# Kernel tuning notes

Hardware: AMD Instinct MI355X
Metric: run time of the kernel (lower is better)

## Reference

```python
import jax, jax.numpy as jnp
import numpy as np

N_GRAPHS = 128
N_NODES = 512
N = N_GRAPHS * N_NODES      # 65536 total nodes
E = 524288                  # edges (avg degree 8)
F_IN = 4                    # num_features
EMB = 4                     # embedding_dim
HEADS = 4
GDIM = 16                   # GATConv_dim
D = GDIM * HEADS            # 64 = d_model
NHEAD = 2                   # heads // 2
FF = 64                     # ff_hid_dim
OUT = 64                    # output_dim
N_GAT_REST = 3              # gat_layers - 1


def setup_inputs() -> dict:
    key = jax.random.key(0)
    ks = iter(jax.random.split(key, 64))
    def nrm(shape, fan_in):
        return jax.random.normal(next(ks), shape, jnp.float32) / np.float32(np.sqrt(fan_in))
    inp = {}
    inp['x'] = jax.random.normal(next(ks), (N, F_IN), jnp.float32)
    inp['edge_index'] = jax.random.randint(next(ks), (2, E), 0, N, dtype=jnp.int32)
    inp['batch'] = jnp.repeat(jnp.arange(N_GRAPHS, dtype=jnp.int32), N_NODES)
    # feature_fc
    inp['Wf'] = nrm((F_IN, EMB), F_IN); inp['bf'] = jnp.zeros((EMB,), jnp.float32)
    # input GATConv (EMB -> HEADS*GDIM)
    inp['gW0'] = nrm((EMB, HEADS * GDIM), EMB)
    inp['aS0'] = nrm((HEADS, GDIM), GDIM); inp['aD0'] = nrm((HEADS, GDIM), GDIM)
    inp['gb0'] = jnp.zeros((D,), jnp.float32)
    # remaining 3 GATConv layers (D -> HEADS*GDIM), stacked
    inp['gW'] = nrm((N_GAT_REST, D, HEADS * GDIM), D)
    inp['aS'] = nrm((N_GAT_REST, HEADS, GDIM), GDIM); inp['aD'] = nrm((N_GAT_REST, HEADS, GDIM), GDIM)
    inp['gb'] = jnp.zeros((N_GAT_REST, D), jnp.float32)
    # decoder layer: self-attn, cross-attn, layernorms, FFN
    for p in ['sWq','sWk','sWv','sWo','cWq','cWk','cWv','cWo']:
        inp[p] = nrm((D, D), D)
    for p in ['sbq','sbk','sbv','sbo','cbq','cbk','cbv','cbo']:
        inp[p] = jnp.zeros((D,), jnp.float32)
    for g, b in [('ln1g','ln1b'), ('ln2g','ln2b'), ('ln3g','ln3b')]:
        inp[g] = jnp.ones((D,), jnp.float32); inp[b] = jnp.zeros((D,), jnp.float32)
    inp['ffW1'] = nrm((D, FF), D); inp['ffb1'] = jnp.zeros((FF,), jnp.float32)
    inp['ffW2'] = nrm((FF, D), FF); inp['ffb2'] = jnp.zeros((D,), jnp.float32)
    inp['fcW'] = nrm((D, OUT), D); inp['fcb'] = jnp.zeros((OUT,), jnp.float32)
    return inp


def _gat(h_in, src, dst, W, a_s, a_d, b):
    # PyG GATConv, concat=True, negative_slope=0.2, self-loops already in (src,dst)
    h = (h_in @ W).reshape(N, HEADS, GDIM)
    es = jnp.einsum('nho,ho->nh', h, a_s)   # [N,H]
    ed = jnp.einsum('nho,ho->nh', h, a_d)
    e = jax.nn.leaky_relu(es[src] + ed[dst], 0.2)          # [E',H]
    m = jax.ops.segment_max(e, dst, num_segments=N)        # segment softmax over dst
    w = jnp.exp(e - m[dst])
    s = jax.ops.segment_sum(w, dst, num_segments=N)
    alpha = w / (s[dst] + 1e-16)
    out = jax.ops.segment_sum(h[src] * alpha[..., None], dst, num_segments=N)
    return out.reshape(N, D) + b


def _mha(q, kv, Wq, bq, Wk, bk, Wv, bv, Wo, bo):
    B, S, Dm = q.shape
    hd = Dm // NHEAD
    Q = (q @ Wq + bq).reshape(B, S, NHEAD, hd)
    K = (kv @ Wk + bk).reshape(B, S, NHEAD, hd)
    V = (kv @ Wv + bv).reshape(B, S, NHEAD, hd)
    a = jax.nn.softmax(jnp.einsum('bqhd,bkhd->bhqk', Q, K) / jnp.sqrt(jnp.float32(hd)), axis=-1)
    o = jnp.einsum('bhqk,bkhd->bqhd', a, V).reshape(B, S, Dm)
    return o @ Wo + bo


def _ln(x, g, b):
    m = x.mean(-1, keepdims=True)
    v = ((x - m) ** 2).mean(-1, keepdims=True)
    return (x - m) / jnp.sqrt(v + 1e-5) * g + b


def reference(x, edge_index, batch, Wf, bf, gW0, aS0, aD0, gb0, gW, aS, aD, gb,
              sWq, sWk, sWv, sWo, cWq, cWk, cWv, cWo,
              sbq, sbk, sbv, sbo, cbq, cbk, cbv, cbo,
              ln1g, ln1b, ln2g, ln2b, ln3g, ln3b,
              ffW1, ffb1, ffW2, ffb2, fcW, fcb):
    loops = jnp.arange(N, dtype=edge_index.dtype)
    src = jnp.concatenate([edge_index[0], loops])
    dst = jnp.concatenate([edge_index[1], loops])
    h = x @ Wf + bf
    h = jax.nn.leaky_relu(_gat(h, src, dst, gW0, aS0, aD0, gb0), 0.01)
    for i in range(N_GAT_REST):
        h = jax.nn.leaky_relu(_gat(h, src, dst, gW[i], aS[i], aD[i], gb[i]), 0.01)
    t = h.reshape(N_GRAPHS, N_NODES, D)
    # one transformer decoder layer, post-norm, memory = layer input
    mem = t
    t = _ln(t + _mha(t, t, sWq, sbq, sWk, sbk, sWv, sbv, sWo, sbo), ln1g, ln1b)
    t = _ln(t + _mha(t, mem, cWq, cbq, cWk, cbk, cWv, cbv, cWo, cbo), ln2g, ln2b)
    t = _ln(t + (jax.nn.relu(t @ ffW1 + ffb1) @ ffW2 + ffb2), ln3g, ln3b)
    h = t.reshape(N, D)
    pooled = jax.ops.segment_sum(h, batch, num_segments=N_GRAPHS) / jnp.float32(N_NODES)
    return pooled @ fcW + fcb
```

## Files before the change

kernel.cpp:

```cpp
#include <hip/hip_runtime.h>
#include <math.h>

#define NG 128
#define SEQ 512
#define NN 65536
#define EE 524288
#define DM 64
#define HSTR 80

typedef __attribute__((ext_vector_type(8))) short short8;
typedef __attribute__((ext_vector_type(4))) short short4v;
typedef __attribute__((ext_vector_type(4))) float f32x4;

__device__ __forceinline__ float lrelu(float x, float s){ return x > 0.f ? x : s*x; }

__device__ __forceinline__ unsigned short f2bf(float x){
  union { float f; unsigned u; } v; v.f = x;
  unsigned r = v.u + 0x7FFF + ((v.u>>16)&1);
  return (unsigned short)(r>>16);
}
__device__ __forceinline__ float bf2f(unsigned short x){
  union { unsigned u; float f; } v; v.u = ((unsigned)x)<<16;
  return v.f;
}

__global__ void k_count(const int* __restrict__ dst, int* __restrict__ deg){
  int e = blockIdx.x*256 + threadIdx.x;
  atomicAdd(&deg[dst[e]], 1);
}

__global__ void k_scan1(const int* __restrict__ deg, int* __restrict__ excl, int* __restrict__ bsums){
  __shared__ int sm[256];
  int tid = threadIdx.x;
  int i = blockIdx.x*256 + tid;
  int v = deg[i];
  sm[tid] = v;
  __syncthreads();
  int val = v;
  for (int off=1; off<256; off<<=1){
    int add = (tid>=off)? sm[tid-off] : 0;
    __syncthreads();
    val += add;
    sm[tid] = val;
    __syncthreads();
  }
  excl[i] = val - v;
  if (tid==255) bsums[blockIdx.x] = val;
}

__global__ void k_scan2(int* __restrict__ bsums){
  __shared__ int sm[256];
  int tid=threadIdx.x;
  int v = bsums[tid];
  sm[tid]=v;
  __syncthreads();
  int val=v;
  for (int off=1; off<256; off<<=1){
    int add = (tid>=off)? sm[tid-off]:0;
    __syncthreads();
    val += add;
    sm[tid]=val;
    __syncthreads();
  }
  bsums[tid] = val - v;
}

__global__ void k_scan3(const int* __restrict__ excl, const int* __restrict__ bsums,
                        int* __restrict__ rowp, int* __restrict__ cursor){
  int i = blockIdx.x*256 + threadIdx.x;
  int v = excl[i] + bsums[blockIdx.x];
  rowp[i]=v; cursor[i]=v;
  if (i==0) rowp[NN]=EE;
}

__global__ void k_fill(const int* __restrict__ src, const int* __restrict__ dst,
                       int* __restrict__ cursor, int* __restrict__ col){
  int e = blockIdx.x*256 + threadIdx.x;
  int d = dst[e];
  int p = atomicAdd(&cursor[d], 1);
  col[p] = src[e];
}

__global__ void __launch_bounds__(256) k_transform0(const float* __restrict__ x,
                            const float* __restrict__ Wf, const float* __restrict__ bf,
                            const float* __restrict__ gW0,
                            const float* __restrict__ aSp, const float* __restrict__ aDp,
                            unsigned short* __restrict__ hout, float* __restrict__ ed){
  __shared__ float inL[4][68];
  __shared__ float Wl[4][64];
  __shared__ float b0l[64];
  __shared__ float asl[64], adl[64];
  int tid = threadIdx.x;
  int n0 = blockIdx.x*64;
  if (tid < 64){
    asl[tid] = aSp[tid]; adl[tid] = aDp[tid];
    float b = 0.f;
    #pragma unroll
    for (int k=0;k<4;k++) b += bf[k]*gW0[k*64+tid];
    b0l[tid] = b;
  }
  {
    int i = tid>>6, j = tid&63;
    float s = 0.f;
    #pragma unroll
    for (int k=0;k<4;k++) s += Wf[i*4+k]*gW0[k*64+j];
    Wl[i][j] = s;
  }
  if (tid < 64){
    float4 v = *(const float4*)&x[(size_t)(n0+tid)*4];
    inL[0][tid]=v.x; inL[1][tid]=v.y; inL[2][tid]=v.z; inL[3][tid]=v.w;
  }
  __syncthreads();
  int i = tid>>4, j = tid&15;
  float acc[4][4];
  #pragma unroll
  for (int r=0;r<4;r++){
    #pragma unroll
    for (int c=0;c<4;c++) acc[r][c] = 0.f;
  }
  #pragma unroll
  for (int k=0;k<4;k++){
    float4 av = *(float4*)&inL[k][4*i];
    float4 bv = *(float4*)&Wl[k][4*j];
    float a_[4]={av.x,av.y,av.z,av.w}, b_[4]={bv.x,bv.y,bv.z,bv.w};
    #pragma unroll
    for (int r=0;r<4;r++){
      #pragma unroll
      for (int c=0;c<4;c++) acc[r][c] += a_[r]*b_[c];
    }
  }
  float4 asv = *(float4*)&asl[4*j];
  float4 adv = *(float4*)&adl[4*j];
  float4 bbv = *(float4*)&b0l[4*j];
  float bb[4] = {bbv.x, bbv.y, bbv.z, bbv.w};
  #pragma unroll
  for (int r=0;r<4;r++){
    float y0=acc[r][0]+bb[0], y1=acc[r][1]+bb[1], y2=acc[r][2]+bb[2], y3=acc[r][3]+bb[3];
    int node = n0 + 4*i + r;
    ushort4 hv;
    hv.x=f2bf(y0); hv.y=f2bf(y1); hv.z=f2bf(y2); hv.w=f2bf(y3);
    *(ushort4*)&hout[(size_t)node*HSTR + 4*j] = hv;
    float ps = y0*asv.x + y1*asv.y + y2*asv.z + y3*asv.w;
    float pd = y0*adv.x + y1*adv.y + y2*adv.z + y3*adv.w;
    ps += __shfl_xor(ps,1); ps += __shfl_xor(ps,2);
    pd += __shfl_xor(pd,1); pd += __shfl_xor(pd,2);
    if ((j&3)==0){
      *(float*)&hout[(size_t)node*HSTR + 64 + 2*(j>>2)] = ps;
      ed[(size_t)node*4 + (j>>2)] = pd;
    }
  }
}

__global__ void __launch_bounds__(256) k_transform_bf(const unsigned short* __restrict__ hin, const float* __restrict__ W,
                            const float* __restrict__ aSp, const float* __restrict__ aDp,
                            unsigned short* __restrict__ hout, float* __restrict__ ed){
  __shared__ float inL[64][68];
  __shared__ float Wl[64][64];
  __shared__ float asl[64], adl[64];
  int tid = threadIdx.x;
  int n0 = blockIdx.x*64;
  if (tid < 64){ asl[tid] = aSp[tid]; adl[tid] = aDp[tid]; }
  for (int idx=tid; idx<1024; idx+=256){
    int k = idx>>4, jj = (idx&15)<<2;
    *(float4*)&Wl[k][jj] = *(const float4*)&W[k*64+jj];
  }
  for (int idx=tid; idx<1024; idx+=256){
    int node = idx>>4, kk = (idx&15)<<2;
    ushort4 v = *(const ushort4*)&hin[(size_t)(n0+node)*64 + kk];
    inL[kk][node]=bf2f(v.x); inL[kk+1][node]=bf2f(v.y); inL[kk+2][node]=bf2f(v.z); inL[kk+3][node]=bf2f(v.w);
  }
  __syncthreads();
  int i = tid>>4, j = tid&15;
  float acc[4][4];
  #pragma unroll
  for (int r=0;r<4;r++){
    #pragma unroll
    for (int c=0;c<4;c++) acc[r][c] = 0.f;
  }
  #pragma unroll 4
  for (int k=0;k<64;k++){
    float4 av = *(float4*)&inL[k][4*i];
    float4 bv = *(float4*)&Wl[k][4*j];
    float a_[4]={av.x,av.y,av.z,av.w}, b_[4]={bv.x,bv.y,bv.z,bv.w};
    #pragma unroll
    for (int r=0;r<4;r++){
      #pragma unroll
      for (int c=0;c<4;c++) acc[r][c] += a_[r]*b_[c];
    }
  }
  float4 asv = *(float4*)&asl[4*j];
  float4 adv = *(float4*)&adl[4*j];
  #pragma unroll
  for (int r=0;r<4;r++){
    float y0=acc[r][0], y1=acc[r][1], y2=acc[r][2], y3=acc[r][3];
    int node = n0 + 4*i + r;
    ushort4 hv;
    hv.x=f2bf(y0); hv.y=f2bf(y1); hv.z=f2bf(y2); hv.w=f2bf(y3);
    *(ushort4*)&hout[(size_t)node*HSTR + 4*j] = hv;
    float ps = y0*asv.x + y1*asv.y + y2*asv.z + y3*asv.w;
    float pd = y0*adv.x + y1*adv.y + y2*adv.z + y3*adv.w;
    ps += __shfl_xor(ps,1); ps += __shfl_xor(ps,2);
    pd += __shfl_xor(pd,1); pd += __shfl_xor(pd,2);
    if ((j&3)==0){
      *(float*)&hout[(size_t)node*HSTR + 64 + 2*(j>>2)] = ps;
      ed[(size_t)node*4 + (j>>2)] = pd;
    }
  }
}

template<int BF16OUT>
__global__ void __launch_bounds__(256) k_aggregate(const unsigned short* __restrict__ h,
                            const float* __restrict__ ed, const int* __restrict__ rowp,
                            const int* __restrict__ col, const float* __restrict__ gb,
                            void* __restrict__ houtv){
  int tid = threadIdx.x;
  int n = blockIdx.x*4 + (tid>>6);
  int l = tid&63;
  int q = l>>4;
  int sl = l&15;
  int head = sl>>2;
  float edn = ed[(size_t)n*4 + head];
  float es_self = *(const float*)&h[(size_t)n*HSTR + 64 + 2*head];
  int beg = __builtin_amdgcn_readfirstlane(rowp[n]);
  int end = __builtin_amdgcn_readfirstlane(rowp[n+1]);
  float m = -1e30f, s = 0.f;
  float a0=0.f, a1=0.f, a2=0.f, a3=0.f;
  int i = beg;
  for (; i+8 <= end; i += 8){
    int c0=col[i], c1=col[i+1], c2=col[i+2], c3=col[i+3];
    int c4=col[i+4], c5=col[i+5], c6=col[i+6], c7=col[i+7];
    int t01 = (q&1)? c1 : c0;
    int t23 = (q&1)? c3 : c2;
    int sq0 = (q&2)? t23 : t01;
    int t45 = (q&1)? c5 : c4;
    int t67 = (q&1)? c7 : c6;
    int sq1 = (q&2)? t67 : t45;
    size_t b0r = (size_t)sq0*HSTR, b1r = (size_t)sq1*HSTR;
    ushort4 hv0 = *(const ushort4*)&h[b0r + 4*sl];
    ushort4 hv1 = *(const ushort4*)&h[b1r + 4*sl];
    float e0 = lrelu(*(const float*)&h[b0r + 64 + 2*head] + edn, 0.2f);
    float e1 = lrelu(*(const float*)&h[b1r + 64 + 2*head] + edn, 0.2f);
    float mx = fmaxf(e0, e1);
    if (__any(mx > m + 8.f)){
      float nm = fmaxf(m, mx);
      float c = __expf(m - nm);
      s*=c; a0*=c; a1*=c; a2*=c; a3*=c; m = nm;
    }
    float w0 = __expf(e0 - m);
    float w1 = __expf(e1 - m);
    s += w0 + w1;
    a0 += w0*bf2f(hv0.x) + w1*bf2f(hv1.x);
    a1 += w0*bf2f(hv0.y) + w1*bf2f(hv1.y);
    a2 += w0*bf2f(hv0.z) + w1*bf2f(hv1.z);
    a3 += w0*bf2f(hv0.w) + w1*bf2f(hv1.w);
  }
  if (i < end){
    int last = end-1;
    int i1=(i+1<last)?i+1:last, i2=(i+2<last)?i+2:last, i3=(i+3<last)?i+3:last;
    int i4=(i+4<last)?i+4:last, i5=(i+5<last)?i+5:last, i6=(i+6<last)?i+6:last;
    int c0=col[i], c1=col[i1], c2=col[i2], c3=col[i3];
    int c4=col[i4], c5=col[i5], c6=col[i6], c7=col[last];
    int t01 = (q&1)? c1 : c0;
    int t23 = (q&1)? c3 : c2;
    int sq0 = (q&2)? t23 : t01;
    int t45 = (q&1)? c5 : c4;
    int t67 = (q&1)? c7 : c6;
    int sq1 = (q&2)? t67 : t45;
    bool ac0 = (i + q) < end;
    bool ac1 = (i + 4 + q) < end;
    size_t b0r = (size_t)sq0*HSTR, b1r = (size_t)sq1*HSTR;
    ushort4 hv0 = *(const ushort4*)&h[b0r + 4*sl];
    ushort4 hv1 = *(const ushort4*)&h[b1r + 4*sl];
    float e0 = lrelu(*(const float*)&h[b0r + 64 + 2*head] + edn, 0.2f);
    float e1 = lrelu(*(const float*)&h[b1r + 64 + 2*head] + edn, 0.2f);
    if (!ac0) e0 = -1e30f;
    if (!ac1) e1 = -1e30f;
    float mx = fmaxf(e0, e1);
    if (__any(mx > m + 8.f)){
      float nm = fmaxf(m, mx);
      float c = __expf(m - nm);
      s*=c; a0*=c; a1*=c; a2*=c; a3*=c; m = nm;
    }
    float w0 = ac0 ? __expf(e0 - m) : 0.f;
    float w1 = ac1 ? __expf(e1 - m) : 0.f;
    s += w0 + w1;
    a0 += w0*bf2f(hv0.x) + w1*bf2f(hv1.x);
    a1 += w0*bf2f(hv0.y) + w1*bf2f(hv1.y);
    a2 += w0*bf2f(hv0.z) + w1*bf2f(hv1.z);
    a3 += w0*bf2f(hv0.w) + w1*bf2f(hv1.w);
  }
  #pragma unroll
  for (int off=16; off<=32; off<<=1){
    float m2 = __shfl_xor(m, off);
    float s2 = __shfl_xor(s, off);
    float b0 = __shfl_xor(a0, off);
    float b1 = __shfl_xor(a1, off);
    float b2 = __shfl_xor(a2, off);
    float b3 = __shfl_xor(a3, off);
    float nm = fmaxf(m, m2);
    float c1 = __expf(m - nm), c2 = __expf(m2 - nm);
    s  = s*c1  + s2*c2;
    a0 = a0*c1 + b0*c2;
    a1 = a1*c1 + b1*c2;
    a2 = a2*c1 + b2*c2;
    a3 = a3*c1 + b3*c2;
    m = nm;
  }
  {
    float e_self = lrelu(es_self + edn, 0.2f);
    float nm = fmaxf(m, e_self);
    float c = __expf(m - nm), cs = __expf(e_self - nm);
    ushort4 hs = *(const ushort4*)&h[(size_t)n*HSTR + 4*sl];
    s  = s*c  + cs;
    a0 = a0*c + cs*bf2f(hs.x);
    a1 = a1*c + cs*bf2f(hs.y);
    a2 = a2*c + cs*bf2f(hs.z);
    a3 = a3*c + cs*bf2f(hs.w);
  }
  if (q == 0){
    float inv = 1.f/(s + 1e-16f);
    float4 gv = *(const float4*)&gb[4*sl];
    float o0 = lrelu(a0*inv + gv.x, 0.01f);
    float o1 = lrelu(a1*inv + gv.y, 0.01f);
    float o2 = lrelu(a2*inv + gv.z, 0.01f);
    float o3 = lrelu(a3*inv + gv.w, 0.01f);
    if (BF16OUT){
      ushort4 hv; hv.x=f2bf(o0); hv.y=f2bf(o1); hv.z=f2bf(o2); hv.w=f2bf(o3);
      *(ushort4*)((unsigned short*)houtv + (size_t)n*64 + 4*sl) = hv;
    } else {
      *(float4*)((float*)houtv + (size_t)n*64 + 4*sl) = make_float4(o0,o1,o2,o3);
    }
  }
}

__global__ void __launch_bounds__(256) k_qkv3(const float* __restrict__ in0, const float* __restrict__ W0, const float* __restrict__ b0, unsigned short* __restrict__ o0,
                      const float* __restrict__ in1, const float* __restrict__ W1, const float* __restrict__ b1, unsigned short* __restrict__ o1,
                      const float* __restrict__ in2, const float* __restrict__ W2, const float* __restrict__ b2, unsigned short* __restrict__ o2,
                      float scl0){
  __shared__ float inL[64][68];
  __shared__ float Wl[64][64];
  int tid = threadIdx.x;
  int n0 = blockIdx.x*64;
  int i = tid>>4, j = tid&15;
  const float* ins[3] = {in0, in1, in2};
  const float* Ws[3] = {W0, W1, W2};
  const float* bs[3] = {b0, b1, b2};
  unsigned short* os[3] = {o0, o1, o2};
  const float* cur = nullptr;
  for (int w=0; w<3; w++){
    __syncthreads();
    if (ins[w] != cur){
      cur = ins[w];
      for (int idx=tid; idx<1024; idx+=256){
        int node = idx>>4, kk = (idx&15)<<2;
        float4 v = *(const float4*)&cur[(size_t)(n0+node)*64 + kk];
        inL[kk][node]=v.x; inL[kk+1][node]=v.y; inL[kk+2][node]=v.z; inL[kk+3][node]=v.w;
      }
    }
    for (int idx=tid; idx<1024; idx+=256){
      int k = idx>>4, jj = (idx&15)<<2;
      *(float4*)&Wl[k][jj] = *(const float4*)&Ws[w][k*64+jj];
    }
    __syncthreads();
    float acc[4][4];
    #pragma unroll
    for (int r=0;r<4;r++){
      #pragma unroll
      for (int c=0;c<4;c++) acc[r][c] = 0.f;
    }
    #pragma unroll 4
    for (int k=0;k<64;k++){
      float4 av = *(float4*)&inL[k][4*i];
      float4 bv = *(float4*)&Wl[k][4*j];
      float a_[4]={av.x,av.y,av.z,av.w}, b_[4]={bv.x,bv.y,bv.z,bv.w};
      #pragma unroll
      for (int r=0;r<4;r++){
        #pragma unroll
        for (int c=0;c<4;c++) acc[r][c] += a_[r]*b_[c];
      }
    }
    float4 bv = *(const float4*)&bs[w][4*j];
    float bb[4] = {bv.x, bv.y, bv.z, bv.w};
    float sc = (w==0) ? scl0 : 1.f;
    #pragma unroll
    for (int r=0;r<4;r++){
      ushort4 hv;
      hv.x = f2bf((acc[r][0]+bb[0])*sc);
      hv.y = f2bf((acc[r][1]+bb[1])*sc);
      hv.z = f2bf((acc[r][2]+bb[2])*sc);
      hv.w = f2bf((acc[r][3]+bb[3])*sc);
      *(ushort4*)&os[w][(size_t)(n0+4*i+r)*64 + 4*j] = hv;
    }
  }
}

__global__ void __launch_bounds__(256) k_ffn(const float* __restrict__ in,
                     const float* __restrict__ W1p, const float* __restrict__ b1p,
                     const float* __restrict__ W2p, const float* __restrict__ b2p,
                     const float* __restrict__ g, const float* __restrict__ bl,
                     float* __restrict__ out){
  __shared__ float inL[64][68];
  __shared__ float Wl[64][64];
  __shared__ float ffL[64][68];
  int tid = threadIdx.x;
  int n0 = blockIdx.x*64;
  for (int idx=tid; idx<1024; idx+=256){
    int k = idx>>4, jj = (idx&15)<<2;
    *(float4*)&Wl[k][jj] = *(const float4*)&W1p[k*64+jj];
  }
  for (int idx=tid; idx<1024; idx+=256){
    int node = idx>>4, kk = (idx&15)<<2;
    float4 v = *(const float4*)&in[(size_t)(n0+node)*64 + kk];
    inL[kk][node]=v.x; inL[kk+1][node]=v.y; inL[kk+2][node]=v.z; inL[kk+3][node]=v.w;
  }
  __syncthreads();
  int i = tid>>4, j = tid&15;
  float acc[4][4];
  #pragma unroll
  for (int r=0;r<4;r++){
    #pragma unroll
    for (int c=0;c<4;c++) acc[r][c] = 0.f;
  }
  #pragma unroll 4
  for (int k=0;k<64;k++){
    float4 av = *(float4*)&inL[k][4*i];
    float4 bv = *(float4*)&Wl[k][4*j];
    float a_[4]={av.x,av.y,av.z,av.w}, b_[4]={bv.x,bv.y,bv.z,bv.w};
    #pragma unroll
    for (int r=0;r<4;r++){
      #pragma unroll
      for (int c=0;c<4;c++) acc[r][c] += a_[r]*b_[c];
    }
  }
  float4 b1v = *(const float4*)&b1p[4*j];
  float bb1[4] = {b1v.x, b1v.y, b1v.z, b1v.w};
  #pragma unroll
  for (int r=0;r<4;r++){
    #pragma unroll
    for (int c=0;c<4;c++){
      ffL[4*j+c][4*i+r] = fmaxf(acc[r][c] + bb1[c], 0.f);
    }
  }
  __syncthreads();
  for (int idx=tid; idx<1024; idx+=256){
    int k = idx>>4, jj = (idx&15)<<2;
    *(float4*)&Wl[k][jj] = *(const float4*)&W2p[k*64+jj];
  }
  __syncthreads();
  #pragma unroll
  for (int r=0;r<4;r++){
    #pragma unroll
    for (int c=0;c<4;c++) acc[r][c] = 0.f;
  }
  #pragma unroll 4
  for (int k=0;k<64;k++){
    float4 av = *(float4*)&ffL[k][4*i];
    float4 bv = *(float4*)&Wl[k][4*j];
    float a_[4]={av.x,av.y,av.z,av.w}, b_[4]={bv.x,bv.y,bv.z,bv.w};
    #pragma unroll
    for (int r=0;r<4;r++){
      #pragma unroll
      for (int c=0;c<4;c++) acc[r][c] += a_[r]*b_[c];
    }
  }
  float4 b2v = *(const float4*)&b2p[4*j];
  float bb2v[4] = {b2v.x, b2v.y, b2v.z, b2v.w};
  float4 gv = *(const float4*)&g[4*j];
  float4 blv = *(const float4*)&bl[4*j];
  float gg[4] = {gv.x, gv.y, gv.z, gv.w};
  float bbl[4] = {blv.x, blv.y, blv.z, blv.w};
  #pragma unroll
  for (int r=0;r<4;r++){
    int node = n0 + 4*i + r;
    float y[4];
    #pragma unroll
    for (int c=0;c<4;c++) y[c] = acc[r][c] + bb2v[c] + inL[4*j+c][4*i+r];
    float s = (y[0]+y[1]) + (y[2]+y[3]);
    s += __shfl_xor(s,1); s += __shfl_xor(s,2); s += __shfl_xor(s,4); s += __shfl_xor(s,8);
    float mean = s * (1.f/64.f);
    float d[4] = {y[0]-mean, y[1]-mean, y[2]-mean, y[3]-mean};
    float v = (d[0]*d[0]+d[1]*d[1]) + (d[2]*d[2]+d[3]*d[3]);
    v += __shfl_xor(v,1); v += __shfl_xor(v,2); v += __shfl_xor(v,4); v += __shfl_xor(v,8);
    float inv = rsqrtf(v*(1.f/64.f) + 1e-5f);
    *(float4*)&out[(size_t)node*64 + 4*j] =
      make_float4(d[0]*inv*gg[0]+bbl[0], d[1]*inv*gg[1]+bbl[1],
                  d[2]*inv*gg[2]+bbl[2], d[3]*inv*gg[3]+bbl[3]);
  }
}

__global__ void __launch_bounds__(512) k_attn_fused(const unsigned short* __restrict__ Q, const unsigned short* __restrict__ K,
                      const unsigned short* __restrict__ V,
                      const float* __restrict__ Wo, const float* __restrict__ bo,
                      const float* __restrict__ res, const float* __restrict__ g, const float* __restrict__ bl,
                      float* __restrict__ out){
  __shared__ __align__(16) char smem[40960];
  char* Ksm = smem;
  char* Vsm = smem + 16384;
  char* Psm = smem + 32768;

  int bid = blockIdx.x;
  int qq = bid & 3;
  int b  = bid >> 2;
  int tid = threadIdx.x;
  int wave = tid>>6;
  int l = tid & 63;
  int lq = l & 15;
  int g4 = l >> 4;
  int head = wave & 1;
  int qg = wave >> 1;
  const size_t gb = (size_t)b*SEQ*64;
  const int hoff = head*32;
  const f32x4 zero = {0.f,0.f,0.f,0.f};

  int qrow0 = qq*128 + qg*32;
  short8 qf[2];
  f32x4 O[2][2];
  float m_[2], l_[2];
  #pragma unroll
  for (int qt=0; qt<2; qt++){
    qf[qt] = *(const short8*)(Q + gb + (size_t)(qrow0 + qt*16 + lq)*64 + hoff + g4*8);
    O[qt][0] = zero; O[qt][1] = zero;
    m_[qt] = -1e30f; l_[qt] = 0.f;
  }
  char* Pw = Psm + wave*1024;

  for (int ph=0; ph<4; ph++){
    __syncthreads();
    #pragma unroll
    for (int it=0; it<2; it++){
      int idx = tid + it*512;
      int row = idx>>3, gr = idx&7;
      uint4 v = *(const uint4*)(K + gb + (size_t)(ph*128 + row)*64 + gr*8);
      *(uint4*)(Ksm + row*128 + ((gr*16) ^ ((row&7)<<4))) = v;
    }
    #pragma unroll
    for (int it=0; it<2; it++){
      int idx = tid + it*512;
      int key = idx>>3, gr = idx&7;
      uint4 vv = *(const uint4*)(V + gb + (size_t)(ph*128 + key)*64 + gr*8);
      const unsigned short* vs = (const unsigned short*)&vv;
      #pragma unroll
      for (int c=0;c<8;c++){
        int d = gr*8 + c;
        *(unsigned short*)(Vsm + d*256 + ((key*2) ^ ((d&7)<<4))) = vs[c];
      }
    }
    __syncthreads();
    for (int p=0; p<4; p++){
      int r0 = p*32 + lq, r1 = r0 + 16;
      short8 kf0 = *(short8*)(Ksm + r0*128 + ((hoff*2 + g4*16) ^ ((r0&7)<<4)));
      short8 kf1 = *(short8*)(Ksm + r1*128 + ((hoff*2 + g4*16) ^ ((r1&7)<<4)));
      int d0 = hoff + lq, d1 = hoff + lq + 16;
      short8 vt0 = *(short8*)(Vsm + d0*256 + ((p*64 + g4*16) ^ ((d0&7)<<4)));
      short8 vt1 = *(short8*)(Vsm + d1*256 + ((p*64 + g4*16) ^ ((d1&7)<<4)));
      int swzp = ((lq>>1)&3)<<4;
      #pragma unroll
      for (int qt=0; qt<2; qt++){
        f32x4 s0 = __builtin_amdgcn_mfma_f32_16x16x32_bf16(kf0, qf[qt], zero, 0,0,0);
        f32x4 s1 = __builtin_amdgcn_mfma_f32_16x16x32_bf16(kf1, qf[qt], zero, 0,0,0);
        float pmax = fmaxf(fmaxf(fmaxf(s0.x,s0.y),fmaxf(s0.z,s0.w)),
                           fmaxf(fmaxf(s1.x,s1.y),fmaxf(s1.z,s1.w)));
        pmax = fmaxf(pmax, __shfl_xor(pmax, 16));
        pmax = fmaxf(pmax, __shfl_xor(pmax, 32));
        float mn = fmaxf(m_[qt], pmax);
        float corr = __expf(m_[qt] - mn);
        m_[qt] = mn;
        float e0 = __expf(s0.x - mn), e1 = __expf(s0.y - mn);
        float e2 = __expf(s0.z - mn), e3 = __expf(s0.w - mn);
        float e4 = __expf(s1.x - mn), e5 = __expf(s1.y - mn);
        float e6 = __expf(s1.z - mn), e7 = __expf(s1.w - mn);
        l_[qt] = l_[qt]*corr + (((e0+e1)+(e2+e3)) + ((e4+e5)+(e6+e7)));
        O[qt][0] *= corr; O[qt][1] *= corr;
        uint2 w0, w1;
        w0.x = (unsigned)f2bf(e0) | ((unsigned)f2bf(e1)<<16);
        w0.y = (unsigned)f2bf(e2) | ((unsigned)f2bf(e3)<<16);
        w1.x = (unsigned)f2bf(e4) | ((unsigned)f2bf(e5)<<16);
        w1.y = (unsigned)f2bf(e6) | ((unsigned)f2bf(e7)<<16);
        *(uint2*)(Pw + lq*64 + ((g4*8) ^ swzp)) = w0;
        *(uint2*)(Pw + lq*64 + ((32 + g4*8) ^ swzp)) = w1;
        short8 pb = *(short8*)(Pw + lq*64 + ((g4*16) ^ swzp));
        O[qt][0] = __builtin_amdgcn_mfma_f32_16x16x32_bf16(vt0, pb, O[qt][0], 0,0,0);
        O[qt][1] = __builtin_amdgcn_mfma_f32_16x16x32_bf16(vt1, pb, O[qt][1], 0,0,0);
      }
    }
  }
  __syncthreads();
  unsigned short* OT = (unsigned short*)smem;
  float* WoL = (float*)(smem + 17664);
  #pragma unroll
  for (int qt=0; qt<2; qt++){
    float lt = l_[qt];
    lt += __shfl_xor(lt, 16);
    lt += __shfl_xor(lt, 32);
    float inv = 1.f/lt;
    int row = qg*32 + qt*16 + lq;
    #pragma unroll
    for (int c=0;c<4;c++){
      OT[(hoff + g4*4 + c)*136 + row]      = f2bf(O[qt][0][c]*inv);
      OT[(hoff + 16 + g4*4 + c)*136 + row] = f2bf(O[qt][1][c]*inv);
    }
  }
  for (int idx=tid; idx<1024; idx+=512){
    int k = idx>>4, jj = (idx&15)<<2;
    *(float4*)&WoL[k*64+jj] = *(const float4*)&Wo[k*64+jj];
  }
  __syncthreads();
  int i = tid>>4, j = tid&15;
  float acc[4][4];
  #pragma unroll
  for (int r=0;r<4;r++){
    #pragma unroll
    for (int c=0;c<4;c++) acc[r][c] = 0.f;
  }
  #pragma unroll 4
  for (int k=0;k<64;k++){
    short4v av = *(short4v*)&OT[k*136 + 4*i];
    float4 bv = *(float4*)&WoL[k*64 + 4*j];
    float b_[4]={bv.x,bv.y,bv.z,bv.w};
    #pragma unroll
    for (int r=0;r<4;r++){
      float a = bf2f((unsigned short)av[r]);
      #pragma unroll
      for (int c=0;c<4;c++) acc[r][c] += a*b_[c];
    }
  }
  float4 bov = *(const float4*)&bo[4*j];
  float4 gv = *(const float4*)&g[4*j];
  float4 blv = *(const float4*)&bl[4*j];
  float bb[4] = {bov.x, bov.y, bov.z, bov.w};
  float gg[4] = {gv.x, gv.y, gv.z, gv.w};
  float bbl[4] = {blv.x, blv.y, blv.z, blv.w};
  #pragma unroll
  for (int r=0;r<4;r++){
    int row = 4*i + r;
    int node = b*SEQ + qq*128 + row;
    float4 rv = *(const float4*)&res[(size_t)node*64 + 4*j];
    float y[4] = {acc[r][0]+bb[0]+rv.x, acc[r][1]+bb[1]+rv.y,
                  acc[r][2]+bb[2]+rv.z, acc[r][3]+bb[3]+rv.w};
    float s = (y[0]+y[1]) + (y[2]+y[3]);
    s += __shfl_xor(s,1); s += __shfl_xor(s,2); s += __shfl_xor(s,4); s += __shfl_xor(s,8);
    float mean = s * (1.f/64.f);
    float d[4] = {y[0]-mean, y[1]-mean, y[2]-mean, y[3]-mean};
    float v = (d[0]*d[0]+d[1]*d[1]) + (d[2]*d[2]+d[3]*d[3]);
    v += __shfl_xor(v,1); v += __shfl_xor(v,2); v += __shfl_xor(v,4); v += __shfl_xor(v,8);
    float inv = rsqrtf(v*(1.f/64.f) + 1e-5f);
    *(float4*)&out[(size_t)node*64 + 4*j] =
      make_float4(d[0]*inv*gg[0]+bbl[0], d[1]*inv*gg[1]+bbl[1],
                  d[2]*inv*gg[2]+bbl[2], d[3]*inv*gg[3]+bbl[3]);
  }
}

__global__ void __launch_bounds__(256) k_pool_fc(const float* __restrict__ t, const float* __restrict__ fcW,
                          const float* __restrict__ fcb, float* __restrict__ out){
  __shared__ float pl[4][64];
  __shared__ float pf[64];
  int b = blockIdx.x;
  int tid = threadIdx.x;
  int j = tid&63, seg = tid>>6;
  const float* basep = t + (size_t)b*SEQ*64;
  float s = 0.f;
  for (int si=seg*128; si<(seg+1)*128; si++) s += basep[(size_t)si*64 + j];
  pl[seg][j] = s;
  __syncthreads();
  if (tid < 64){
    pf[tid] = (pl[0][tid]+pl[1][tid]+pl[2][tid]+pl[3][tid]) * (1.f/512.f);
  }
  __syncthreads();
  if (tid < 64){
    float o = fcb[tid];
    for (int k=0;k<64;k++) o += pf[k]*fcW[k*64+tid];
    out[(size_t)b*64 + tid] = o;
  }
}

extern "C" void kernel_launch(void* const* d_in, const int* in_sizes, int n_in,
                              void* d_out, int out_size, void* d_ws, size_t ws_size,
                              hipStream_t stream) {
  const float* x    = (const float*)d_in[0];
  const int*   ei   = (const int*)d_in[1];
  const float* Wf   = (const float*)d_in[3];
  const float* bf   = (const float*)d_in[4];
  const float* gW0  = (const float*)d_in[5];
  const float* aS0  = (const float*)d_in[6];
  const float* aD0  = (const float*)d_in[7];
  const float* gb0  = (const float*)d_in[8];
  const float* gW   = (const float*)d_in[9];
  const float* aS   = (const float*)d_in[10];
  const float* aD   = (const float*)d_in[11];
  const float* gb   = (const float*)d_in[12];
  const float* sWq  = (const float*)d_in[13];
  const float* sWk  = (const float*)d_in[14];
  const float* sWv  = (const float*)d_in[15];
  const float* sWo  = (const float*)d_in[16];
  const float* cWq  = (const float*)d_in[17];
  const float* cWk  = (const float*)d_in[18];
  const float* cWv  = (const float*)d_in[19];
  const float* cWo  = (const float*)d_in[20];
  const float* sbq  = (const float*)d_in[21];
  const float* sbk  = (const float*)d_in[22];
  const float* sbv  = (const float*)d_in[23];
  const float* sbo  = (const float*)d_in[24];
  const float* cbq  = (const float*)d_in[25];
  const float* cbk  = (const float*)d_in[26];
  const float* cbv  = (const float*)d_in[27];
  const float* cbo  = (const float*)d_in[28];
  const float* ln1g = (const float*)d_in[29];
  const float* ln1b = (const float*)d_in[30];
  const float* ln2g = (const float*)d_in[31];
  const float* ln2b = (const float*)d_in[32];
  const float* ln3g = (const float*)d_in[33];
  const float* ln3b = (const float*)d_in[34];
  const float* ffW1 = (const float*)d_in[35];
  const float* ffb1 = (const float*)d_in[36];
  const float* ffW2 = (const float*)d_in[37];
  const float* ffb2 = (const float*)d_in[38];
  const float* fcW  = (const float*)d_in[39];
  const float* fcb  = (const float*)d_in[40];

  char* ws = (char*)d_ws;
  size_t off = 0;
  auto alloc = [&](size_t bytes) -> void* {
    void* p = ws + off;
    off += (bytes + 255) & ~(size_t)255;
    return p;
  };
  int* deg    = (int*)alloc(NN*sizeof(int));
  int* excl   = (int*)alloc(NN*sizeof(int));
  int* rowp   = (int*)alloc((NN+1)*sizeof(int));
  int* cursor = (int*)alloc(NN*sizeof(int));
  int* col    = (int*)alloc(EE*sizeof(int));
  int* bsums  = (int*)alloc(256*sizeof(int));
  float* ed   = (float*)alloc((size_t)NN*4*sizeof(float));
  unsigned short* Hb   = (unsigned short*)alloc((size_t)NN*HSTR*sizeof(unsigned short));
  unsigned short* Hagg = (unsigned short*)alloc((size_t)NN*64*sizeof(unsigned short));
  unsigned short* Qb = (unsigned short*)alloc((size_t)NN*64*sizeof(unsigned short));
  unsigned short* Kb = (unsigned short*)alloc((size_t)NN*64*sizeof(unsigned short));
  unsigned short* Vb = (unsigned short*)alloc((size_t)NN*64*sizeof(unsigned short));
  float* B1   = (float*)alloc((size_t)NN*64*sizeof(float));
  float* B2   = (float*)alloc((size_t)NN*64*sizeof(float));
  float* B5   = (float*)alloc((size_t)NN*64*sizeof(float));

  const int* e_src = ei;
  const int* e_dst = ei + EE;

  const float scale = 0.17677669529663687f;

  hipMemsetAsync(deg, 0, NN*sizeof(int), stream);
  k_count<<<EE/256, 256, 0, stream>>>(e_dst, deg);
  k_scan1<<<NN/256, 256, 0, stream>>>(deg, excl, bsums);
  k_scan2<<<1, 256, 0, stream>>>(bsums);
  k_scan3<<<NN/256, 256, 0, stream>>>(excl, bsums, rowp, cursor);
  k_fill<<<EE/256, 256, 0, stream>>>(e_src, e_dst, cursor, col);

  k_transform0<<<NN/64, 256, 0, stream>>>(x, Wf, bf, gW0, aS0, aD0, Hb, ed);
  k_aggregate<1><<<NN/4, 256, 0, stream>>>(Hb, ed, rowp, col, gb0, Hagg);
  k_transform_bf<<<NN/64, 256, 0, stream>>>(Hagg, gW+0*4096, aS+0*64, aD+0*64, Hb, ed);
  k_aggregate<1><<<NN/4, 256, 0, stream>>>(Hb, ed, rowp, col, gb+0*64, Hagg);
  k_transform_bf<<<NN/64, 256, 0, stream>>>(Hagg, gW+1*4096, aS+1*64, aD+1*64, Hb, ed);
  k_aggregate<1><<<NN/4, 256, 0, stream>>>(Hb, ed, rowp, col, gb+1*64, Hagg);
  k_transform_bf<<<NN/64, 256, 0, stream>>>(Hagg, gW+2*4096, aS+2*64, aD+2*64, Hb, ed);
  k_aggregate<0><<<NN/4, 256, 0, stream>>>(Hb, ed, rowp, col, gb+2*64, B2);

  k_qkv3<<<NN/64, 256, 0, stream>>>(B2, sWq, sbq, Qb, B2, sWk, sbk, Kb, B2, sWv, sbv, Vb, scale);
  k_attn_fused<<<NG*4, 512, 0, stream>>>(Qb, Kb, Vb, sWo, sbo, B2, ln1g, ln1b, B5);

  k_qkv3<<<NN/64, 256, 0, stream>>>(B5, cWq, cbq, Qb, B2, cWk, cbk, Kb, B2, cWv, cbv, Vb, scale);
  k_attn_fused<<<NG*4, 512, 0, stream>>>(Qb, Kb, Vb, cWo, cbo, B5, ln2g, ln2b, B2);

  k_ffn<<<NN/64, 256, 0, stream>>>(B2, ffW1, ffb1, ffW2, ffb2, ln3g, ln3b, B1);

  k_pool_fc<<<NG, 256, 0, stream>>>(B1, fcW, fcb, (float*)d_out);
}
```

Before: 409.1 us.

## Process 64-key blocks per softmax step with lazy max rescaling and new V swizzle

The flash-attention inner loop now handles 64 keys per online-softmax step instead of 32. This halves the number of max reductions and rescales. Rescaling of the running max is skipped unless some lane's new max exceeds the old one by more than 8, which removes most correction exps and multiplies. The V transpose swizzle and the P staging buffer are changed to reduce LDS bank conflicts, at the cost of more shared memory (48KB) and more live registers, which may lower occupancy.

Result: no change. 409.0 us (-0.0%).

```diff
diff --git a/kernel.cpp b/kernel.cpp
--- a/kernel.cpp
+++ b/kernel.cpp
@@ -493,7 +493,7 @@
                       const float* __restrict__ Wo, const float* __restrict__ bo,
                       const float* __restrict__ res, const float* __restrict__ g, const float* __restrict__ bl,
                       float* __restrict__ out){
-  __shared__ __align__(16) char smem[40960];
+  __shared__ __align__(16) char smem[49152];
   char* Ksm = smem;
   char* Vsm = smem + 16384;
   char* Psm = smem + 32768;
@@ -522,7 +522,11 @@
     O[qt][0] = zero; O[qt][1] = zero;
     m_[qt] = -1e30f; l_[qt] = 0.f;
   }
-  char* Pw = Psm + wave*1024;
+  char* Pw = Psm + wave*2048;
+  int swzp = (lq&7)<<4;
+  int d0 = hoff + lq, d1 = hoff + lq + 16;
+  int sv0 = (((d0&7) ^ ((d0>>3)&7)) << 4);
+  int sv1 = (((d1&7) ^ ((d1>>3)&7)) << 4);
 
   for (int ph=0; ph<4; ph++){
     __syncthreads();
@@ -542,45 +546,69 @@
       #pragma unroll
       for (int c=0;c<8;c++){
         int d = gr*8 + c;
-        *(unsigned short*)(Vsm + d*256 + ((key*2) ^ ((d&7)<<4))) = vs[c];
+        int swz = ((c ^ gr) & 7) << 4;
+        *(unsigned short*)(Vsm + d*256 + ((key*2) ^ swz)) = vs[c];
       }
     }
     __syncthreads();
-    for (int p=0; p<4; p++){
-      int r0 = p*32 + lq, r1 = r0 + 16;
-      short8 kf0 = *(short8*)(Ksm + r0*128 + ((hoff*2 + g4*16) ^ ((r0&7)<<4)));
-      short8 kf1 = *(short8*)(Ksm + r1*128 + ((hoff*2 + g4*16) ^ ((r1&7)<<4)));
-      int d0 = hoff + lq, d1 = hoff + lq + 16;
-      short8 vt0 = *(short8*)(Vsm + d0*256 + ((p*64 + g4*16) ^ ((d0&7)<<4)));
-      short8 vt1 = *(short8*)(Vsm + d1*256 + ((p*64 + g4*16) ^ ((d1&7)<<4)));
-      int swzp = ((lq>>1)&3)<<4;
+    for (int p2=0; p2<2; p2++){
+      int rb = p2*64 + lq;
+      short8 kf0 = *(short8*)(Ksm + rb*128      + ((hoff*2 + g4*16) ^ ((rb&7)<<4)));
+      short8 kf1 = *(short8*)(Ksm + (rb+16)*128 + ((hoff*2 + g4*16) ^ (((rb+16)&7)<<4)));
+      short8 kf2 = *(short8*)(Ksm + (rb+32)*128 + ((hoff*2 + g4*16) ^ (((rb+32)&7)<<4)));
+      short8 kf3 = *(short8*)(Ksm + (rb+48)*128 + ((hoff*2 + g4*16) ^ (((rb+48)&7)<<4)));
+      short8 vt00 = *(short8*)(Vsm + d0*256 + ((p2*128 + g4*16) ^ sv0));
+      short8 vt01 = *(short8*)(Vsm + d0*256 + ((p2*128 + 64 + g4*16) ^ sv0));
+      short8 vt10 = *(short8*)(Vsm + d1*256 + ((p2*128 + g4*16) ^ sv1));
+      short8 vt11 = *(short8*)(Vsm + d1*256 + ((p2*128 + 64 + g4*16) ^ sv1));
       #pragma unroll
       for (int qt=0; qt<2; qt++){
         f32x4 s0 = __builtin_amdgcn_mfma_f32_16x16x32_bf16(kf0, qf[qt], zero, 0,0,0);
         f32x4 s1 = __builtin_amdgcn_mfma_f32_16x16x32_bf16(kf1, qf[qt], zero, 0,0,0);
-        float pmax = fmaxf(fmaxf(fmaxf(s0.x,s0.y),fmaxf(s0.z,s0.w)),
-                           fmaxf(fmaxf(s1.x,s1.y),fmaxf(s1.z,s1.w)));
+        f32x4 s2 = __builtin_amdgcn_mfma_f32_16x16x32_bf16(kf2, qf[qt], zero, 0,0,0);
+        f32x4 s3 = __builtin_amdgcn_mfma_f32_16x16x32_bf16(kf3, qf[qt], zero, 0,0,0);
+        float pmax = fmaxf(
+          fmaxf(fmaxf(fmaxf(s0.x,s0.y),fmaxf(s0.z,s0.w)), fmaxf(fmaxf(s1.x,s1.y),fmaxf(s1.z,s1.w))),
+          fmaxf(fmaxf(fmaxf(s2.x,s2.y),fmaxf(s2.z,s2.w)), fmaxf(fmaxf(s3.x,s3.y),fmaxf(s3.z,s3.w))));
         pmax = fmaxf(pmax, __shfl_xor(pmax, 16));
         pmax = fmaxf(pmax, __shfl_xor(pmax, 32));
-        float mn = fmaxf(m_[qt], pmax);
-        float corr = __expf(m_[qt] - mn);
-        m_[qt] = mn;
-        float e0 = __expf(s0.x - mn), e1 = __expf(s0.y - mn);
-        float e2 = __expf(s0.z - mn), e3 = __expf(s0.w - mn);
-        float e4 = __expf(s1.x - mn), e5 = __expf(s1.y - mn);
-        float e6 = __expf(s1.z - mn), e7 = __expf(s1.w - mn);
-        l_[qt] = l_[qt]*corr + (((e0+e1)+(e2+e3)) + ((e4+e5)+(e6+e7)));
-        O[qt][0] *= corr; O[qt][1] *= corr;
-        uint2 w0, w1;
+        if (__any(pmax > m_[qt] + 8.f)){
+          float mn = fmaxf(m_[qt], pmax);
+          float corr = __expf(m_[qt] - mn);
+          l_[qt] *= corr;
+          O[qt][0] *= corr; O[qt][1] *= corr;
+          m_[qt] = mn;
+        }
+        float mm = m_[qt];
+        float e0 = __expf(s0.x - mm), e1 = __expf(s0.y - mm);
+        float e2 = __expf(s0.z - mm), e3 = __expf(s0.w - mm);
+        float e4 = __expf(s1.x - mm), e5 = __expf(s1.y - mm);
+        float e6 = __expf(s1.z - mm), e7 = __expf(s1.w - mm);
+        float e8 = __expf(s2.x - mm), e9 = __expf(s2.y - mm);
+        float ea = __expf(s2.z - mm), eb = __expf(s2.w - mm);
+        float ec = __expf(s3.x - mm), ed_ = __expf(s3.y - mm);
+        float ee = __expf(s3.z - mm), ef = __expf(s3.w - mm);
+        l_[qt] += (((e0+e1)+(e2+e3)) + ((e4+e5)+(e6+e7)))
+                + (((e8+e9)+(ea+eb)) + ((ec+ed_)+(ee+ef)));
+        uint2 w0, w1, w2, w3;
         w0.x = (unsigned)f2bf(e0) | ((unsigned)f2bf(e1)<<16);
         w0.y = (unsigned)f2bf(e2) | ((unsigned)f2bf(e3)<<16);
         w1.x = (unsigned)f2bf(e4) | ((unsigned)f2bf(e5)<<16);
         w1.y = (unsigned)f2bf(e6) | ((unsigned)f2bf(e7)<<16);
-        *(uint2*)(Pw + lq*64 + ((g4*8) ^ swzp)) = w0;
-        *(uint2*)(Pw + lq*64 + ((32 + g4*8) ^ swzp)) = w1;
-        short8 pb = *(short8*)(Pw + lq*64 + ((g4*16) ^ swzp));
-        O[qt][0] = __builtin_amdgcn_mfma_f32_16x16x32_bf16(vt0, pb, O[qt][0], 0,0,0);
-        O[qt][1] = __builtin_amdgcn_mfma_f32_16x16x32_bf16(vt1, pb, O[qt][1], 0,0,0);
+        w2.x = (unsigned)f2bf(e8) | ((unsigned)f2bf(e9)<<16);
+        w2.y = (unsigned)f2bf(ea) | ((unsigned)f2bf(eb)<<16);
+        w3.x = (unsigned)f2bf(ec) | ((unsigned)f2bf(ed_)<<16);
+        w3.y = (unsigned)f2bf(ee) | ((unsigned)f2bf(ef)<<16);
+        *(uint2*)(Pw + lq*128 + ((g4*8) ^ swzp))      = w0;
+        *(uint2*)(Pw + lq*128 + ((32 + g4*8) ^ swzp)) = w1;
+        *(uint2*)(Pw + lq*128 + ((64 + g4*8) ^ swzp)) = w2;
+        *(uint2*)(Pw + lq*128 + ((96 + g4*8) ^ swzp)) = w3;
+        short8 pb0 = *(short8*)(Pw + lq*128 + ((g4*16) ^ swzp));
+        short8 pb1 = *(short8*)(Pw + lq*128 + ((64 + g4*16) ^ swzp));
+        O[qt][0] = __builtin_amdgcn_mfma_f32_16x16x32_bf16(vt00, pb0, O[qt][0], 0,0,0);
+        O[qt][0] = __builtin_amdgcn_mfma_f32_16x16x32_bf16(vt01, pb1, O[qt][0], 0,0,0);
+        O[qt][1] = __builtin_amdgcn_mfma_f32_16x16x32_bf16(vt10, pb0, O[qt][1], 0,0,0);
+        O[qt][1] = __builtin_amdgcn_mfma_f32_16x16x32_bf16(vt11, pb1, O[qt][1], 0,0,0);
       }
     }
   }
```
